# Performance work log

Measured on AMD Instinct MI355X. Metric: run time of the kernel, lower is better.

## Reference

```python
import jax, jax.numpy as jnp
import numpy as np

B, H, W = 8, 64, 64
DIM, NH, WS = 768, 12, 14
HD = DIM // NH            # head dim = 64
N = WS * WS               # tokens per window = 196
PAD = (WS - H % WS) % WS  # 6 -> padded grid 70
HP, WP = H + PAD, W + PAD
NW = (HP // WS) * (WP // WS)  # 25 windows
EPS = 1e-5


def _layer_norm(x, w, b):
    mu = x.mean(-1, keepdims=True)
    var = ((x - mu) ** 2).mean(-1, keepdims=True)
    return (x - mu) * jax.lax.rsqrt(var + EPS) * w + b


def _window_partition(x):
    # [B,H,W,C] -> [B*NW, WS, WS, C] with zero padding
    x = jnp.pad(x, ((0, 0), (0, PAD), (0, PAD), (0, 0)))
    x = x.reshape(B, HP // WS, WS, WP // WS, WS, DIM)
    return x.transpose(0, 1, 3, 2, 4, 5).reshape(-1, WS, WS, DIM)


def _window_unpartition(w):
    x = w.reshape(B, HP // WS, WP // WS, WS, WS, DIM)
    x = x.transpose(0, 1, 3, 2, 4, 5).reshape(B, HP, WP, DIM)
    return x[:, :H, :W, :]


def _rel_table(rel_pos):
    # get_rel_pos with q_size==k_size==WS, rel_pos already (2*WS-1, HD):
    # Rh[i,j] = rel_pos[i - j + WS - 1]; summed over channel dim (batched_index_and_sum sums last dim)
    coords = jnp.arange(WS)[:, None] - jnp.arange(WS)[None, :] + (WS - 1)
    return rel_pos[coords].sum(-1)  # (WS, WS)


def _attention(w, q_idx, k_idx, qkv_w, qkv_b, proj_w, proj_b, rel_h, rel_w):
    Bp = w.shape[0]  # B*NW
    xq = w.reshape(Bp, N, DIM)
    qkv = xq @ qkv_w + qkv_b                                  # (Bp, N, 3*DIM)
    qkv = qkv.reshape(Bp, N, 3, NH, HD).transpose(2, 0, 3, 1, 4)
    qkv = qkv.reshape(3, Bp * NH, N, HD)
    q, k, v = qkv[0], qkv[1], qkv[2]
    scale = HD ** -0.5
    attn = jnp.einsum('bqc,bkc->bqk', q * scale, k)           # (Bp*NH, N, N)
    # decomposed rel-pos bias via irregular per-batch index gather
    Sh, Sw = _rel_table(rel_h), _rel_table(rel_w)
    qr, qc = q_idx // WS, q_idx % WS                          # (Bp*NH, N)
    kr, kc = k_idx // WS, k_idx % WS
    bias = Sh[qr[:, :, None], kr[:, None, :]] + Sw[qc[:, :, None], kc[:, None, :]]
    attn = jax.nn.softmax(attn + bias, axis=-1)
    out = jnp.einsum('bqk,bkc->bqc', attn, v)                 # (Bp*NH, N, HD)
    out = out.reshape(Bp, NH, N, HD).transpose(0, 2, 1, 3).reshape(Bp, WS, WS, DIM)
    return out @ proj_w + proj_b


def _block(x, q_idx, k_idx, ln1_w, ln1_b, ln2_w, ln2_b, qkv_w, qkv_b,
           proj_w, proj_b, rel_h, rel_w, mlp_w1, mlp_b1, mlp_w2, mlp_b2):
    shortcut = x
    h = _layer_norm(x, ln1_w, ln1_b)
    win = _window_partition(h)
    win = _attention(win, q_idx, k_idx, qkv_w, qkv_b, proj_w, proj_b, rel_h, rel_w)
    h = _window_unpartition(win)
    x = shortcut + h
    m = _layer_norm(x, ln2_w, ln2_b)
    m = jax.nn.gelu(m @ mlp_w1 + mlp_b1, approximate=False) @ mlp_w2 + mlp_b2
    return x + m


def setup_inputs() -> dict:
    key = jax.random.key(0)
    ks = jax.random.split(key, 12)
    f = lambda k, s: jax.random.normal(k, s, jnp.float32) * 0.02
    return {
        'x': jax.random.normal(ks[0], (B, H, W, DIM), jnp.float32),
        'q_idx': jnp.sort(jax.random.randint(ks[1], (B * NW * NH, N), 0, N), axis=-1),
        'k_idx': jnp.sort(jax.random.randint(ks[2], (B * NW * NH, N), 0, N), axis=-1),
        'ln1_w': jnp.ones((DIM,), jnp.float32), 'ln1_b': jnp.zeros((DIM,), jnp.float32),
        'ln2_w': jnp.ones((DIM,), jnp.float32), 'ln2_b': jnp.zeros((DIM,), jnp.float32),
        'qkv_w': f(ks[3], (DIM, 3 * DIM)), 'qkv_b': jnp.zeros((3 * DIM,), jnp.float32),
        'proj_w': f(ks[4], (DIM, DIM)), 'proj_b': jnp.zeros((DIM,), jnp.float32),
        'rel_h': f(ks[5], (2 * WS - 1, HD)), 'rel_w': f(ks[6], (2 * WS - 1, HD)),
        'mlp_w1': f(ks[7], (DIM, 4 * DIM)), 'mlp_b1': jnp.zeros((4 * DIM,), jnp.float32),
        'mlp_w2': f(ks[8], (4 * DIM, DIM)), 'mlp_b2': jnp.zeros((DIM,), jnp.float32),
    }


def reference(x, q_idx, k_idx, ln1_w, ln1_b, ln2_w, ln2_b, qkv_w, qkv_b,
              proj_w, proj_b, rel_h, rel_w, mlp_w1, mlp_b1, mlp_w2, mlp_b2):
    return _block(x, q_idx, k_idx, ln1_w, ln1_b, ln2_w, ln2_b, qkv_w, qkv_b,
                  proj_w, proj_b, rel_h, rel_w, mlp_w1, mlp_b1, mlp_w2, mlp_b2)
```

## Files before the change

kernel.cpp:

```cpp
#include <hip/hip_runtime.h>


typedef __bf16 bf16x8 __attribute__((ext_vector_type(8)));
typedef float f32x4 __attribute__((ext_vector_type(4)));
typedef unsigned int u32x4 __attribute__((ext_vector_type(4)));

__device__ __forceinline__ unsigned short f2bf(float f) {
  unsigned int u = __builtin_bit_cast(unsigned int, f);
  u += 0x7FFFu + ((u >> 16) & 1u);
  return (unsigned short)(u >> 16);
}

__device__ __forceinline__ bf16x8 ld8(const unsigned short* p) {
  return __builtin_bit_cast(bf16x8, *(const u32x4*)p);
}

__device__ __forceinline__ void gload_lds16(const unsigned short* g,
                                            unsigned short* l) {
  __builtin_amdgcn_global_load_lds(
      (const __attribute__((address_space(1))) unsigned int*)g,
      (__attribute__((address_space(3))) unsigned int*)l, 16, 0, 0);
}

__global__ void transpose_w(const float* __restrict__ in,
                            unsigned short* __restrict__ out, int K, int N) {
  __shared__ float t[32][33];
  int n = blockIdx.x * 32 + threadIdx.x;
  int kb = blockIdx.y * 32;
#pragma unroll
  for (int i = 0; i < 4; i++) {
    int k = kb + threadIdx.y + i * 8;
    t[threadIdx.y + i * 8][threadIdx.x] = in[(size_t)k * N + n];
  }
  __syncthreads();
  int k2 = kb + threadIdx.x;
#pragma unroll
  for (int i = 0; i < 4; i++) {
    int n2 = blockIdx.x * 32 + threadIdx.y + i * 8;
    out[(size_t)n2 * K + k2] = f2bf(t[threadIdx.x][threadIdx.y + i * 8]);
  }
}

__global__ void shsw_kernel(const float* __restrict__ rh,
                            const float* __restrict__ rw,
                            float* __restrict__ o) {
  int t = threadIdx.x;
  if (t < 196) {
    int i = t / 14, j = t % 14, d = i - j + 13;
    float sh = 0.f, sw = 0.f;
    for (int c = 0; c < 64; c++) {
      sh += rh[d * 64 + c];
      sw += rw[d * 64 + c];
    }
    o[t] = sh;
    o[196 + t] = sw;
  }
}

__global__ __launch_bounds__(256) void ln_kernel(
    const float* __restrict__ xin, const float* __restrict__ w,
    const float* __restrict__ b, unsigned short* __restrict__ out,
    int windowed) {
  __shared__ float red[8];
  __shared__ float ms[2];
  const int tid = threadIdx.x;
  const int blk = blockIdx.x;
  const float* xr = xin + (size_t)blk * 768;
  float v0 = xr[tid], v1 = xr[tid + 256], v2 = xr[tid + 512];
  float s = v0 + v1 + v2;
  float q = v0 * v0 + v1 * v1 + v2 * v2;
#pragma unroll
  for (int off = 32; off > 0; off >>= 1) {
    s += __shfl_down(s, off, 64);
    q += __shfl_down(q, off, 64);
  }
  const int wv = tid >> 6, lane = tid & 63;
  if (lane == 0) { red[wv] = s; red[4 + wv] = q; }
  __syncthreads();
  if (tid == 0) {
    float st = red[0] + red[1] + red[2] + red[3];
    float qt = red[4] + red[5] + red[6] + red[7];
    float mu = st * (1.0f / 768.0f);
    float var = qt * (1.0f / 768.0f) - mu * mu;
    ms[0] = mu;
    ms[1] = rsqrtf(var + 1e-5f);
  }
  __syncthreads();
  float mu = ms[0], sc = ms[1];
  unsigned short* dst;
  if (windowed) {
    int bb = blk >> 12, rem = blk & 4095, h = rem >> 6, ww = rem & 63;
    int win = (bb * 5 + h / 14) * 5 + ww / 14;
    int t = (h % 14) * 14 + (ww % 14);
    dst = out + ((size_t)win * 196 + t) * 768;
  } else {
    dst = out + (size_t)blk * 768;
  }
  dst[tid] = f2bf((v0 - mu) * sc * w[tid] + b[tid]);
  dst[tid + 256] = f2bf((v1 - mu) * sc * w[tid + 256] + b[tid + 256]);
  dst[tid + 512] = f2bf((v2 - mu) * sc * w[tid + 512] + b[tid + 512]);
}

template <int EPI>
__global__ __launch_bounds__(256, 2) void gemm_bt(
    const unsigned short* __restrict__ A, const unsigned short* __restrict__ Bt,
    const float* __restrict__ bias, int M, int N, int K,
    unsigned short* __restrict__ obf, float* __restrict__ of,
    const float* __restrict__ resid) {
  __shared__ __align__(16) unsigned short As[128 * 32];
  __shared__ __align__(16) unsigned short Bs[128 * 32];
  const int tid = threadIdx.x;
  const int lane = tid & 63, wv = tid >> 6;
  const int ln15 = lane & 15, quad = lane >> 4;
  const int wm = wv & 1, wn = wv >> 1;

  int bid = blockIdx.y * gridDim.x + blockIdx.x;
  {
    const int nwg = gridDim.x * gridDim.y;
    const int q = nwg >> 3, r = nwg & 7;
    const int xcd = bid & 7, lo = bid >> 3;
    bid = (xcd < r ? xcd * (q + 1) : r * (q + 1) + (xcd - r) * q) + lo;
  }
  const int m0 = (bid / gridDim.x) * 128, n0 = (bid % gridDim.x) * 128;

  const int ra0 = tid >> 2, ka0 = (tid & 3) * 8;
  const unsigned short* pA0 = A + (size_t)min(m0 + ra0, M - 1) * K + ka0;
  const unsigned short* pA1 = A + (size_t)min(m0 + ra0 + 64, M - 1) * K + ka0;
  const unsigned short* pB0 = Bt + (size_t)(n0 + ra0) * K + ka0;
  const unsigned short* pB1 = Bt + (size_t)(n0 + ra0 + 64) * K + ka0;
  unsigned short* lA0 = As + tid * 8;
  unsigned short* lA1 = As + 2048 + tid * 8;
  unsigned short* lB0 = Bs + tid * 8;
  unsigned short* lB1 = Bs + 2048 + tid * 8;

  const f32x4 fz = {0.f, 0.f, 0.f, 0.f};
  f32x4 acc[4][4];
#pragma unroll
  for (int i = 0; i < 4; i++)
#pragma unroll
    for (int j = 0; j < 4; j++) acc[i][j] = fz;

  for (int kt = 0; kt < K; kt += 32) {
    __syncthreads();
    gload_lds16(pA0 + kt, lA0);
    gload_lds16(pA1 + kt, lA1);
    gload_lds16(pB0 + kt, lB0);
    gload_lds16(pB1 + kt, lB1);
    __syncthreads();
    bf16x8 af[4], bv[4];
#pragma unroll
    for (int t = 0; t < 4; t++) {
      af[t] = ld8(As + (wm * 64 + t * 16 + ln15) * 32 + quad * 8);
      bv[t] = ld8(Bs + (wn * 64 + t * 16 + ln15) * 32 + quad * 8);
    }
#pragma unroll
    for (int i = 0; i < 4; i++)
#pragma unroll
      for (int j = 0; j < 4; j++)
        acc[i][j] =
            __builtin_amdgcn_mfma_f32_16x16x32_bf16(af[i], bv[j], acc[i][j], 0, 0, 0);
  }

#pragma unroll
  for (int i = 0; i < 4; i++) {
#pragma unroll
    for (int j = 0; j < 4; j++) {
      const int col = n0 + wn * 64 + j * 16 + ln15;
      const float bc = bias[col];
#pragma unroll
      for (int g = 0; g < 4; g++) {
        const int row = m0 + wm * 64 + i * 16 + quad * 4 + g;
        if (row >= M) continue;
        float v = acc[i][j][g] + bc;
        if constexpr (EPI == 0) {
          obf[(size_t)row * N + col] = f2bf(v);
        } else if constexpr (EPI == 2) {
          float gl = 0.5f * v * (1.0f + erff(v * 0.70710678118f));
          obf[(size_t)row * N + col] = f2bf(gl);
        } else if constexpr (EPI == 1) {
          int win = row / 196, t = row - win * 196;
          int b = win / 25, wg = win - b * 25;
          int wr = wg / 5, wc = wg - wr * 5;
          int h = wr * 14 + t / 14;
          int w = wc * 14 + (t % 14);
          if (h < 64 && w < 64) {
            size_t oi = (((size_t)(b * 64 + h)) * 64 + w) * 768 + col;
            of[oi] = v + resid[oi];
          }
        } else {
          size_t oi = (size_t)row * N + col;
          of[oi] += v;
        }
      }
    }
  }
}

__global__ __launch_bounds__(256, 2) void attn_kernel(
    const unsigned short* __restrict__ qkv, const int* __restrict__ q_idx,
    const int* __restrict__ k_idx, const float* __restrict__ shsw,
    unsigned short* __restrict__ attnout) {
  __shared__ __align__(16) unsigned short Vt[64][232];
  __shared__ __align__(16) unsigned short Pst[4][16 * 232];
  __shared__ float Shs[196], Sws[196];
  __shared__ short qr14a[208], qc14a[208], kra[208], kca[208];

  const int tid = threadIdx.x;
  const int blk = blockIdx.x;
  const int win = blk / 12, head = blk % 12;
  const int lane = tid & 63, wv = tid >> 6;
  const int ln15 = lane & 15, quad = lane >> 4;
  const unsigned short* qg = qkv + (size_t)win * 196 * 2304;

  {
    unsigned int* vz = (unsigned int*)&Vt[0][0];
    for (int i = tid; i < 64 * 232 / 2; i += 256) vz[i] = 0u;
    unsigned int* pz = (unsigned int*)&Pst[0][0];
    for (int i = tid; i < 4 * 16 * 232 / 2; i += 256) pz[i] = 0u;
  }
  for (int i = tid; i < 196 * 64; i += 256) {
    int r = i >> 6, c = i & 63;
    Vt[c][r] = qg[(size_t)r * 2304 + 1536 + head * 64 + c];
  }
  for (int i = tid; i < 208; i += 256) {
    if (i < 196) {
      Shs[i] = shsw[i];
      Sws[i] = shsw[196 + i];
    }
    int q = (i < 196) ? q_idx[(size_t)blk * 196 + i] : 0;
    int k = (i < 196) ? k_idx[(size_t)blk * 196 + i] : 0;
    qr14a[i] = (short)((q / 14) * 14);
    qc14a[i] = (short)((q % 14) * 14);
    kra[i] = (short)(k / 14);
    kca[i] = (short)(k % 14);
  }
  __syncthreads();

  const f32x4 fz = {0.f, 0.f, 0.f, 0.f};
  unsigned short* strip = &Pst[wv][0];

  for (int mt = wv; mt < 13; mt += 4) {
    int qrow = mt * 16 + ln15;
    int qrc = (qrow < 196) ? qrow : 0;
    const unsigned short* qrp = qg + (size_t)qrc * 2304 + head * 64 + quad * 8;
    bf16x8 aq0 = ld8(qrp);
    bf16x8 aq1 = ld8(qrp + 32);

    f32x4 sacc[13];
#pragma unroll
    for (int nt = 0; nt < 13; nt++) {
      sacc[nt] = fz;
      int krow = nt * 16 + ln15;
      if (krow > 195) krow = 0;
      const unsigned short* krp =
          qg + (size_t)krow * 2304 + 768 + head * 64 + quad * 8;
      bf16x8 bk0 = ld8(krp);
      bf16x8 bk1 = ld8(krp + 32);
      sacc[nt] = __builtin_amdgcn_mfma_f32_16x16x32_bf16(aq0, bk0, sacc[nt], 0, 0, 0);
      sacc[nt] = __builtin_amdgcn_mfma_f32_16x16x32_bf16(aq1, bk1, sacc[nt], 0, 0, 0);
    }

    const int r0 = mt * 16 + quad * 4;
    int qi[4], qci[4];
#pragma unroll
    for (int g = 0; g < 4; g++) {
      qi[g] = qr14a[r0 + g];
      qci[g] = qc14a[r0 + g];
    }
    float rmax[4] = {-1e30f, -1e30f, -1e30f, -1e30f};
#pragma unroll
    for (int nt = 0; nt < 13; nt++) {
      int col = nt * 16 + ln15;
      int kr_ = kra[col], kc_ = kca[col];
#pragma unroll
      for (int g = 0; g < 4; g++) {
        float v = sacc[nt][g] * 0.125f + Shs[qi[g] + kr_] + Sws[qci[g] + kc_];
        if (col >= 196) v = -1e30f;
        sacc[nt][g] = v;
        rmax[g] = fmaxf(rmax[g], v);
      }
    }
#pragma unroll
    for (int off = 1; off < 16; off <<= 1)
#pragma unroll
      for (int g = 0; g < 4; g++)
        rmax[g] = fmaxf(rmax[g], __shfl_xor(rmax[g], off, 16));
    float rsum[4] = {0.f, 0.f, 0.f, 0.f};
#pragma unroll
    for (int nt = 0; nt < 13; nt++) {
      int col = nt * 16 + ln15;
#pragma unroll
      for (int g = 0; g < 4; g++) {
        float p = (col >= 196) ? 0.f : __expf(sacc[nt][g] - rmax[g]);
        sacc[nt][g] = p;
        rsum[g] += p;
      }
    }
#pragma unroll
    for (int off = 1; off < 16; off <<= 1)
#pragma unroll
      for (int g = 0; g < 4; g++) rsum[g] += __shfl_xor(rsum[g], off, 16);
    float rinv[4];
#pragma unroll
    for (int g = 0; g < 4; g++) rinv[g] = 1.0f / rsum[g];

#pragma unroll
    for (int nt = 0; nt < 13; nt++) {
      int col = nt * 16 + ln15;
#pragma unroll
      for (int g = 0; g < 4; g++)
        strip[(quad * 4 + g) * 232 + col] = f2bf(sacc[nt][g] * rinv[g]);
    }

    f32x4 oacc[4];
#pragma unroll
    for (int c4 = 0; c4 < 4; c4++) oacc[c4] = fz;
#pragma unroll
    for (int ks = 0; ks < 7; ks++) {
      bf16x8 ap = ld8(strip + ln15 * 232 + ks * 32 + quad * 8);
#pragma unroll
      for (int c4 = 0; c4 < 4; c4++) {
        bf16x8 bvv = ld8(&Vt[c4 * 16 + ln15][ks * 32 + quad * 8]);
        oacc[c4] = __builtin_amdgcn_mfma_f32_16x16x32_bf16(ap, bvv, oacc[c4], 0, 0, 0);
      }
    }
#pragma unroll
    for (int c4 = 0; c4 < 4; c4++)
#pragma unroll
      for (int g = 0; g < 4; g++) {
        int row = r0 + g;
        if (row < 196)
          attnout[((size_t)win * 196 + row) * 768 + head * 64 + c4 * 16 + ln15] =
              f2bf(oacc[c4][g]);
      }
  }
}

extern "C" void kernel_launch(void* const* d_in, const int* in_sizes, int n_in,
                              void* d_out, int out_size, void* d_ws,
                              size_t ws_size, hipStream_t stream) {
  const float* x = (const float*)d_in[0];
  const int* q_idx = (const int*)d_in[1];
  const int* k_idx = (const int*)d_in[2];
  const float* ln1w = (const float*)d_in[3];
  const float* ln1b = (const float*)d_in[4];
  const float* ln2w = (const float*)d_in[5];
  const float* ln2b = (const float*)d_in[6];
  const float* qkvw = (const float*)d_in[7];
  const float* qkvb = (const float*)d_in[8];
  const float* projw = (const float*)d_in[9];
  const float* projb = (const float*)d_in[10];
  const float* relh = (const float*)d_in[11];
  const float* relw = (const float*)d_in[12];
  const float* w1 = (const float*)d_in[13];
  const float* b1 = (const float*)d_in[14];
  const float* w2 = (const float*)d_in[15];
  const float* b2 = (const float*)d_in[16];
  float* out = (float*)d_out;

  char* ws = (char*)d_ws;
  unsigned short* xw = (unsigned short*)ws;
  const size_t offA = 60211200;
  unsigned short* qkv = (unsigned short*)(ws + offA);
  const size_t offB = offA + 201326592;
  unsigned short* qkvwt = (unsigned short*)(ws + offB);
  unsigned short* projwt = qkvwt + 2304 * 768;
  unsigned short* w1t = projwt + 768 * 768;
  unsigned short* w2t = w1t + 3072 * 768;
  float* shsw = (float*)(w2t + 768 * 3072);

  unsigned short* attnout = xw;
  unsigned short* ln2buf = xw;
  unsigned short* mlp1 = qkv;

  hipMemsetAsync(xw, 0, (size_t)39200 * 768 * 2, stream);

  dim3 tb(32, 8);
  transpose_w<<<dim3(2304 / 32, 768 / 32), tb, 0, stream>>>(qkvw, qkvwt, 768, 2304);
  transpose_w<<<dim3(768 / 32, 768 / 32), tb, 0, stream>>>(projw, projwt, 768, 768);
  transpose_w<<<dim3(3072 / 32, 768 / 32), tb, 0, stream>>>(w1, w1t, 768, 3072);
  transpose_w<<<dim3(768 / 32, 3072 / 32), tb, 0, stream>>>(w2, w2t, 3072, 768);
  shsw_kernel<<<1, 256, 0, stream>>>(relh, relw, shsw);

  ln_kernel<<<32768, 256, 0, stream>>>(x, ln1w, ln1b, xw, 1);

  gemm_bt<0><<<dim3(18, 307), 256, 0, stream>>>(xw, qkvwt, qkvb, 39200, 2304,
                                                768, qkv, nullptr, nullptr);
  attn_kernel<<<2400, 256, 0, stream>>>(qkv, q_idx, k_idx, shsw, attnout);

  gemm_bt<1><<<dim3(6, 307), 256, 0, stream>>>(attnout, projwt, projb, 39200,
                                               768, 768, nullptr, out, x);
  ln_kernel<<<32768, 256, 0, stream>>>(out, ln2w, ln2b, ln2buf, 0);

  gemm_bt<2><<<dim3(24, 256), 256, 0, stream>>>(ln2buf, w1t, b1, 32768, 3072,
                                                768, mlp1, nullptr, nullptr);
  gemm_bt<3><<<dim3(6, 256), 256, 0, stream>>>(mlp1, w2t, b2, 32768, 768, 3072,
                                               nullptr, out, nullptr);
  (void)in_sizes; (void)n_in; (void)out_size; (void)ws_size;
}
```

Before: 1.267 ms.

## Rewrite GEMM as 256x256 tile, 8-wave, double-buffered pipelined kernel with swizzled LDS

The bf16 GEMM moves from 128x128 tiles with 4 waves and one LDS buffer to 256x256 tiles with 8 waves, BK=64, and a two-buffer LDS scheme of 128KB. Loads for the next tile are staged while the MFMA quarter-tiles run, using explicit barriers, vmcnt waits and setprio. An XOR swizzle on the LDS layout is meant to avoid bank conflicts. The aim is to hide global-load latency and raise data reuse, at the cost of heavy LDS use (about one block per CU), more register pressure, and more tail waste on M=39200.

```diff
diff --git a/kernel.cpp b/kernel.cpp
--- a/kernel.cpp
+++ b/kernel.cpp
@@ -102,13 +102,13 @@
 }
 
 template <int EPI>
-__global__ __launch_bounds__(256, 2) void gemm_bt(
+__global__ __launch_bounds__(512, 2) void gemm_bt(
     const unsigned short* __restrict__ A, const unsigned short* __restrict__ Bt,
     const float* __restrict__ bias, int M, int N, int K,
     unsigned short* __restrict__ obf, float* __restrict__ of,
     const float* __restrict__ resid) {
-  __shared__ __align__(16) unsigned short As[128 * 32];
-  __shared__ __align__(16) unsigned short Bs[128 * 32];
+  __shared__ __align__(16) unsigned short smem[65536];
+
   const int tid = threadIdx.x;
   const int lane = tid & 63, wv = tid >> 6;
   const int ln15 = lane & 15, quad = lane >> 4;
@@ -117,59 +117,139 @@
   int bid = blockIdx.y * gridDim.x + blockIdx.x;
   {
     const int nwg = gridDim.x * gridDim.y;
-    const int q = nwg >> 3, r = nwg & 7;
+    const int qq = nwg >> 3, rr = nwg & 7;
     const int xcd = bid & 7, lo = bid >> 3;
-    bid = (xcd < r ? xcd * (q + 1) : r * (q + 1) + (xcd - r) * q) + lo;
-  }
-  const int m0 = (bid / gridDim.x) * 128, n0 = (bid % gridDim.x) * 128;
-
-  const int ra0 = tid >> 2, ka0 = (tid & 3) * 8;
-  const unsigned short* pA0 = A + (size_t)min(m0 + ra0, M - 1) * K + ka0;
-  const unsigned short* pA1 = A + (size_t)min(m0 + ra0 + 64, M - 1) * K + ka0;
-  const unsigned short* pB0 = Bt + (size_t)(n0 + ra0) * K + ka0;
-  const unsigned short* pB1 = Bt + (size_t)(n0 + ra0 + 64) * K + ka0;
-  unsigned short* lA0 = As + tid * 8;
-  unsigned short* lA1 = As + 2048 + tid * 8;
-  unsigned short* lB0 = Bs + tid * 8;
-  unsigned short* lB1 = Bs + 2048 + tid * 8;
+    bid = (xcd < rr ? xcd * (qq + 1) : rr * (qq + 1) + (xcd - rr) * qq) + lo;
+  }
+  const int m0 = (bid / gridDim.x) * 256, n0 = (bid % gridDim.x) * 256;
+
+  const int r0 = tid >> 3;
+  const int cOff = ((tid & 7) ^ (r0 & 7)) * 8;
+  int rA[4];
+#pragma unroll
+  for (int hq = 0; hq < 4; hq++) rA[hq] = min(m0 + hq * 64 + r0, M - 1);
+  const unsigned short* pB = Bt + (size_t)(n0 + r0) * K + cOff;
+
+  int chnk[2];
+#pragma unroll
+  for (int ks = 0; ks < 2; ks++) chnk[ks] = ((ks * 4 + quad) ^ (ln15 & 7)) * 8;
 
   const f32x4 fz = {0.f, 0.f, 0.f, 0.f};
-  f32x4 acc[4][4];
-#pragma unroll
-  for (int i = 0; i < 4; i++)
+  f32x4 acc[8][4];
+#pragma unroll
+  for (int i = 0; i < 8; i++)
 #pragma unroll
     for (int j = 0; j < 4; j++) acc[i][j] = fz;
 
-  for (int kt = 0; kt < K; kt += 32) {
-    __syncthreads();
-    gload_lds16(pA0 + kt, lA0);
-    gload_lds16(pA1 + kt, lA1);
-    gload_lds16(pB0 + kt, lB0);
-    gload_lds16(pB1 + kt, lB1);
-    __syncthreads();
-    bf16x8 af[4], bv[4];
-#pragma unroll
-    for (int t = 0; t < 4; t++) {
-      af[t] = ld8(As + (wm * 64 + t * 16 + ln15) * 32 + quad * 8);
-      bv[t] = ld8(Bs + (wn * 64 + t * 16 + ln15) * 32 + quad * 8);
-    }
-#pragma unroll
-    for (int i = 0; i < 4; i++)
-#pragma unroll
-      for (int j = 0; j < 4; j++)
-        acc[i][j] =
-            __builtin_amdgcn_mfma_f32_16x16x32_bf16(af[i], bv[j], acc[i][j], 0, 0, 0);
-  }
-
-#pragma unroll
-  for (int i = 0; i < 4; i++) {
+  bf16x8 af[4][2];
+  bf16x8 bf_[2][2][2];
+
+#define STAGE_A(BB, HH, KT)                                                   \
+  do {                                                                        \
+    unsigned short* d_ = smem + (BB)*32768 + (HH)*8192 + tid * 8;             \
+    gload_lds16(A + (size_t)rA[(HH)*2 + 0] * K + cOff + (KT), d_);            \
+    gload_lds16(A + (size_t)rA[(HH)*2 + 1] * K + cOff + (KT), d_ + 4096);     \
+  } while (0)
+#define STAGE_B(BB, HH, KT)                                                   \
+  do {                                                                        \
+    unsigned short* d_ = smem + (BB)*32768 + 16384 + (HH)*8192 + tid * 8;     \
+    gload_lds16(pB + (size_t)((HH)*128) * K + (KT), d_);                      \
+    gload_lds16(pB + (size_t)((HH)*128 + 64) * K + (KT), d_ + 4096);          \
+  } while (0)
+#define LOAD_A(BB, QRH)                                                       \
+  do {                                                                        \
+    const unsigned short* ab_ = smem + (BB)*32768 + wm * 8192;                \
+    _Pragma("unroll") for (int fi = 0; fi < 4; fi++)                          \
+        _Pragma("unroll") for (int ks = 0; ks < 2; ks++)                      \
+            af[fi][ks] =                                                      \
+        ld8(ab_ + ((QRH)*64 + fi * 16 + ln15) * 64 + chnk[ks]);               \
+  } while (0)
+#define LOAD_B(BB, CH)                                                        \
+  do {                                                                        \
+    const unsigned short* bb_ =                                               \
+        smem + (BB)*32768 + 16384 + (wn >> 1) * 8192 + (wn & 1) * 4096;       \
+    _Pragma("unroll") for (int fj = 0; fj < 2; fj++)                          \
+        _Pragma("unroll") for (int ks = 0; ks < 2; ks++)                      \
+            bf_[CH][fj][ks] =                                                 \
+        ld8(bb_ + ((CH)*32 + fj * 16 + ln15) * 64 + chnk[ks]);                \
+  } while (0)
+#define MFMA16(QRH, CH)                                                       \
+  do {                                                                        \
+    _Pragma("unroll") for (int fi = 0; fi < 4; fi++)                          \
+        _Pragma("unroll") for (int fj = 0; fj < 2; fj++)                      \
+            _Pragma("unroll") for (int ks = 0; ks < 2; ks++)                  \
+                acc[(QRH)*4 + fi][(CH)*2 + fj] =                              \
+        __builtin_amdgcn_mfma_f32_16x16x32_bf16(                              \
+            af[fi][ks], bf_[CH][fj][ks], acc[(QRH)*4 + fi][(CH)*2 + fj], 0,   \
+            0, 0);                                                            \
+  } while (0)
+#define BAR() __builtin_amdgcn_s_barrier()
+#define PRIO1 __builtin_amdgcn_s_setprio(1)
+#define PRIO0 __builtin_amdgcn_s_setprio(0)
+
+#define TILE(BB, NB, KT1, KT2, S12, S34, W)                                   \
+  do {                                                                        \
+    LOAD_A(BB, 0);                                                            \
+    LOAD_B(BB, 0);                                                            \
+    if (S12) STAGE_B(NB, 1, KT1);                                             \
+    BAR(); PRIO1; MFMA16(0, 0); PRIO0; BAR();                                 \
+    LOAD_B(BB, 1);                                                            \
+    if (S12) STAGE_A(NB, 1, KT1);                                             \
+    BAR(); PRIO1; MFMA16(0, 1); PRIO0; BAR();                                 \
+    LOAD_A(BB, 1);                                                            \
+    if (S34) STAGE_B(BB, 0, KT2);                                             \
+    BAR(); PRIO1; MFMA16(1, 0); PRIO0; BAR();                                 \
+    if (S34) STAGE_A(BB, 0, KT2);                                             \
+    if ((W) == 0) {                                                           \
+      asm volatile("s_waitcnt vmcnt(4)" ::: "memory");                        \
+      __builtin_amdgcn_sched_barrier(0);                                      \
+    } else if ((W) == 1) {                                                    \
+      asm volatile("s_waitcnt vmcnt(0)" ::: "memory");                        \
+      __builtin_amdgcn_sched_barrier(0);                                      \
+    }                                                                         \
+    BAR(); PRIO1; MFMA16(1, 1); PRIO0; BAR();                                 \
+  } while (0)
+
+  const int NT = K >> 6;
+
+  STAGE_B(0, 0, 0);
+  STAGE_A(0, 0, 0);
+  STAGE_B(0, 1, 0);
+  STAGE_A(0, 1, 0);
+  STAGE_B(1, 0, 64);
+  STAGE_A(1, 0, 64);
+  asm volatile("s_waitcnt vmcnt(4)" ::: "memory");
+  __builtin_amdgcn_sched_barrier(0);
+  BAR();
+
+  int kt = 0;
+  for (int t = 0; t + 3 < NT; t += 2) {
+    TILE(0, 1, kt + 64, kt + 128, 1, 1, 0);
+    TILE(1, 0, kt + 128, kt + 192, 1, 1, 0);
+    kt += 128;
+  }
+  TILE(0, 1, kt + 64, 0, 1, 0, 1);
+  TILE(1, 0, 0, 0, 0, 0, 2);
+
+#undef TILE
+#undef STAGE_A
+#undef STAGE_B
+#undef LOAD_A
+#undef LOAD_B
+#undef MFMA16
+#undef BAR
+#undef PRIO1
+#undef PRIO0
+
+#pragma unroll
+  for (int i = 0; i < 8; i++) {
 #pragma unroll
     for (int j = 0; j < 4; j++) {
       const int col = n0 + wn * 64 + j * 16 + ln15;
       const float bc = bias[col];
 #pragma unroll
       for (int g = 0; g < 4; g++) {
-        const int row = m0 + wm * 64 + i * 16 + quad * 4 + g;
+        const int row = m0 + wm * 128 + i * 16 + quad * 4 + g;
         if (row >= M) continue;
         float v = acc[i][j][g] + bc;
         if constexpr (EPI == 0) {
@@ -384,17 +464,17 @@
 
   ln_kernel<<<32768, 256, 0, stream>>>(x, ln1w, ln1b, xw, 1);
 
-  gemm_bt<0><<<dim3(18, 307), 256, 0, stream>>>(xw, qkvwt, qkvb, 39200, 2304,
-                                                768, qkv, nullptr, nullptr);
+  gemm_bt<0><<<dim3(9, 154), 512, 0, stream>>>(xw, qkvwt, qkvb, 39200, 2304,
+                                               768, qkv, nullptr, nullptr);
   attn_kernel<<<2400, 256, 0, stream>>>(qkv, q_idx, k_idx, shsw, attnout);
 
-  gemm_bt<1><<<dim3(6, 307), 256, 0, stream>>>(attnout, projwt, projb, 39200,
+  gemm_bt<1><<<dim3(3, 154), 512, 0, stream>>>(attnout, projwt, projb, 39200,
                                                768, 768, nullptr, out, x);
   ln_kernel<<<32768, 256, 0, stream>>>(out, ln2w, ln2b, ln2buf, 0);
 
-  gemm_bt<2><<<dim3(24, 256), 256, 0, stream>>>(ln2buf, w1t, b1, 32768, 3072,
+  gemm_bt<2><<<dim3(12, 128), 512, 0, stream>>>(ln2buf, w1t, b1, 32768, 3072,
                                                 768, mlp1, nullptr, nullptr);
-  gemm_bt<3><<<dim3(6, 256), 256, 0, stream>>>(mlp1, w2t, b2, 32768, 768, 3072,
+  gemm_bt<3><<<dim3(3, 128), 512, 0, stream>>>(mlp1, w2t, b2, 32768, 768, 3072,
                                                nullptr, out, nullptr);
   (void)in_sizes; (void)n_in; (void)out_size; (void)ws_size;
 }
```

New measurement: 1.526 ms. 1.2x slower.

## Double-buffer GEMM LDS tiles and swizzle columns to avoid bank conflicts

Applied to the files above, without the earlier changes.

The bf16 GEMM now keeps two LDS buffers and prefetches the next K-tile with global_load_lds while MFMAs run on the current tile. This replaces the two barriers per iteration with a single waitcnt-plus-barrier. The global source column is XOR-swizzled so the fragment reads from LDS hit fewer bank conflicts. LDS use doubles to 32KB per block, which may limit occupancy, and correctness depends on the read-side swizzle matching the write side.

```diff
diff --git a/kernel.cpp b/kernel.cpp
--- a/kernel.cpp
+++ b/kernel.cpp
@@ -107,8 +107,7 @@
     const float* __restrict__ bias, int M, int N, int K,
     unsigned short* __restrict__ obf, float* __restrict__ of,
     const float* __restrict__ resid) {
-  __shared__ __align__(16) unsigned short As[128 * 32];
-  __shared__ __align__(16) unsigned short Bs[128 * 32];
+  __shared__ __align__(16) unsigned short smem[2][8192];
   const int tid = threadIdx.x;
   const int lane = tid & 63, wv = tid >> 6;
   const int ln15 = lane & 15, quad = lane >> 4;
@@ -117,21 +116,22 @@
   int bid = blockIdx.y * gridDim.x + blockIdx.x;
   {
     const int nwg = gridDim.x * gridDim.y;
-    const int q = nwg >> 3, r = nwg & 7;
+    const int qq = nwg >> 3, rr = nwg & 7;
     const int xcd = bid & 7, lo = bid >> 3;
-    bid = (xcd < r ? xcd * (q + 1) : r * (q + 1) + (xcd - r) * q) + lo;
+    bid = (xcd < rr ? xcd * (qq + 1) : rr * (qq + 1) + (xcd - rr) * qq) + lo;
   }
   const int m0 = (bid / gridDim.x) * 128, n0 = (bid % gridDim.x) * 128;
 
-  const int ra0 = tid >> 2, ka0 = (tid & 3) * 8;
-  const unsigned short* pA0 = A + (size_t)min(m0 + ra0, M - 1) * K + ka0;
-  const unsigned short* pA1 = A + (size_t)min(m0 + ra0 + 64, M - 1) * K + ka0;
-  const unsigned short* pB0 = Bt + (size_t)(n0 + ra0) * K + ka0;
-  const unsigned short* pB1 = Bt + (size_t)(n0 + ra0 + 64) * K + ka0;
-  unsigned short* lA0 = As + tid * 8;
-  unsigned short* lA1 = As + 2048 + tid * 8;
-  unsigned short* lB0 = Bs + tid * 8;
-  unsigned short* lB1 = Bs + 2048 + tid * 8;
+  const int rr_ = tid >> 2;
+  const int csrc =
+      (((tid & 3) ^ ((tid >> 2) & 3) ^ (((tid >> 4) & 1) << 1)) << 3);
+  const unsigned short* pA0 = A + (size_t)min(m0 + rr_, M - 1) * K + csrc;
+  const unsigned short* pA1 = A + (size_t)min(m0 + 64 + rr_, M - 1) * K + csrc;
+  const unsigned short* pB0 = Bt + (size_t)(n0 + rr_) * K + csrc;
+  const unsigned short* pB1 = Bt + (size_t)(n0 + 64 + rr_) * K + csrc;
+
+  const int rslot =
+      ((quad ^ (ln15 & 3) ^ (((ln15 >> 2) & 1) << 1)) << 3);
 
   const f32x4 fz = {0.f, 0.f, 0.f, 0.f};
   f32x4 acc[4][4];
@@ -140,18 +140,30 @@
 #pragma unroll
     for (int j = 0; j < 4; j++) acc[i][j] = fz;
 
+#define STAGE(BUF, KT)                                                        \
+  do {                                                                        \
+    unsigned short* d_ = &smem[BUF][0] + tid * 8;                             \
+    gload_lds16(pA0 + (KT), d_);                                              \
+    gload_lds16(pA1 + (KT), d_ + 2048);                                       \
+    gload_lds16(pB0 + (KT), d_ + 4096);                                       \
+    gload_lds16(pB1 + (KT), d_ + 6144);                                       \
+  } while (0)
+
+  STAGE(0, 0);
+  asm volatile("s_waitcnt vmcnt(0)" ::: "memory");
+  __builtin_amdgcn_sched_barrier(0);
+  __builtin_amdgcn_s_barrier();
+
+  int cur = 0;
   for (int kt = 0; kt < K; kt += 32) {
-    __syncthreads();
-    gload_lds16(pA0 + kt, lA0);
-    gload_lds16(pA1 + kt, lA1);
-    gload_lds16(pB0 + kt, lB0);
-    gload_lds16(pB1 + kt, lB1);
-    __syncthreads();
+    const bool more = (kt + 32 < K);
+    if (more) STAGE(cur ^ 1, kt + 32);
     bf16x8 af[4], bv[4];
+    const unsigned short* cb = &smem[cur][0];
 #pragma unroll
     for (int t = 0; t < 4; t++) {
-      af[t] = ld8(As + (wm * 64 + t * 16 + ln15) * 32 + quad * 8);
-      bv[t] = ld8(Bs + (wn * 64 + t * 16 + ln15) * 32 + quad * 8);
+      af[t] = ld8(cb + (wm * 64 + t * 16 + ln15) * 32 + rslot);
+      bv[t] = ld8(cb + 4096 + (wn * 64 + t * 16 + ln15) * 32 + rslot);
     }
 #pragma unroll
     for (int i = 0; i < 4; i++)
@@ -159,7 +171,14 @@
       for (int j = 0; j < 4; j++)
         acc[i][j] =
             __builtin_amdgcn_mfma_f32_16x16x32_bf16(af[i], bv[j], acc[i][j], 0, 0, 0);
-  }
+    if (more) {
+      asm volatile("s_waitcnt vmcnt(0)" ::: "memory");
+      __builtin_amdgcn_sched_barrier(0);
+      __builtin_amdgcn_s_barrier();
+    }
+    cur ^= 1;
+  }
+#undef STAGE
 
 #pragma unroll
   for (int i = 0; i < 4; i++) {
```

After: 1.284 ms. No clear change (+1.3%).
